# Kernel tuning notes

Measured on AMD Instinct MI355X. Metric: run time of the kernel, lower is better.

## Reference

```python
import jax, jax.numpy as jnp
from jax import lax
import numpy as np

INPUT_SIZE = 128
NUM_FRAMES = 4
NUM_OBJECTS = 32
DN = ('NCHW', 'OIHW', 'NCHW')


def _conv(x, w, b):
    y = lax.conv_general_dilated(x, w, window_strides=(1, 1), padding='SAME',
                                 dimension_numbers=DN)
    return y + b[None, :, None, None]


def setup_inputs() -> dict:
    key = jax.random.key(0)
    k = jax.random.split(key, 6)
    B = 32
    images = jax.random.uniform(k[0], (B, NUM_FRAMES, 3, INPUT_SIZE, INPUT_SIZE), jnp.float32) * 255.0
    rois = jax.random.randint(k[1], (B, INPUT_SIZE, INPUT_SIZE), 0, NUM_OBJECTS, jnp.int32)
    conv1_w = jax.random.normal(k[2], (64, 3 * NUM_FRAMES, 3, 3), jnp.float32) * 0.05
    conv1_b = jnp.zeros((64,), jnp.float32)
    conv2_w = jax.random.normal(k[3], (128, 64, 3, 3), jnp.float32) * 0.05
    conv2_b = jnp.zeros((128,), jnp.float32)
    return {'images': images, 'rois': rois, 'conv1_w': conv1_w, 'conv1_b': conv1_b,
            'conv2_w': conv2_w, 'conv2_b': conv2_b}


def reference(images, rois, conv1_w, conv1_b, conv2_w, conv2_b):
    B = images.shape[0]
    # backbone: conv -> relu -> maxpool2x2 -> conv -> relu
    x = images.reshape(B, 3 * NUM_FRAMES, INPUT_SIZE, INPUT_SIZE) / 255.0
    x = jax.nn.relu(_conv(x, conv1_w, conv1_b))
    x = lax.reduce_window(x, -jnp.inf, lax.max, (1, 1, 2, 2), (1, 1, 2, 2), 'VALID')
    x = jax.nn.relu(_conv(x, conv2_w, conv2_b))  # (B, 128, 64, 64)
    C = x.shape[1]
    # roi_pool: one-hot(rois) nearest-downsampled to 64x64, broadcast-multiply,
    # max over H,W == per-id segment max (x >= 0 post-relu; absent id -> 0)
    ids = rois[:, ::2, ::2].reshape(B, -1)
    feat = x.reshape(B, C, -1).transpose(0, 2, 1)  # (B, HW, C)

    def pool_one(f, i):  # f: (HW, C), i: (HW,)
        return jax.ops.segment_max(f, i, num_segments=NUM_OBJECTS)  # (O, C)

    pooled = jax.vmap(pool_one)(feat, ids)  # (B, O, C)
    return jnp.maximum(pooled, 0.0)
```

## Files before the change

kernel.cpp:

```cpp
#include <hip/hip_runtime.h>

#define IN 128
#define PD 64
#define C1 64
#define C2 128
#define ICC 12
#define NOBJ 32
#define PADW 66

typedef __attribute__((ext_vector_type(8))) short bf16x8;
typedef __attribute__((ext_vector_type(4))) float f32x4;

static __device__ __forceinline__ unsigned short f2bf(float f) {
  unsigned u = __float_as_uint(f);
  return (unsigned short)((u + 0x7FFFu + ((u >> 16) & 1u)) >> 16);
}

__global__ __launch_bounds__(256) void k0_pack_w2(
    const float* __restrict__ w2, unsigned short* __restrict__ wq)
{
  int j = blockIdx.x * 256 + threadIdx.x;
  if (j < 9 * 2 * 8 * 64 * 8) {
    const int e   = j & 7;
    const int l15 = (j >> 3) & 15;
    const int l16 = (j >> 7) & 3;
    const int ocb = (j >> 9) & 7;
    const int k2  = (j >> 12) & 1;
    const int tap = j >> 13;
    const int oc = ocb * 16 + l15;
    const int ic = k2 * 32 + l16 * 8 + e;
    wq[j] = f2bf(w2[((size_t)oc * C1 + ic) * 9 + tap]);
  }
}

__global__ __launch_bounds__(256) void k0_pack_w1(
    const float* __restrict__ w1, unsigned short* __restrict__ wp)
{
  int i = blockIdx.x * 256 + threadIdx.x;
  if (i < 10 * C1 * 16) {
    int tap = i >> 10;
    int rem = i & 1023;
    int oc = rem >> 4, ch = rem & 15;
    float v = (tap < 9 && ch < ICC) ? w1[((size_t)oc * ICC + ch) * 9 + tap] : 0.f;
    wp[i] = f2bf(v);
  }
}

__global__ __launch_bounds__(256) void k_border(unsigned short* __restrict__ xpad)
{
  int i = blockIdx.x * 256 + threadIdx.x;
  if (i >= 32 * 260) return;
  int b = i / 260, p = i - b * 260;
  int y, x;
  if (p < 66)       { y = 0;           x = p; }
  else if (p < 132) { y = 65;          x = p - 66; }
  else if (p < 196) { y = p - 132 + 1; x = 0; }
  else              { y = p - 196 + 1; x = 65; }
  unsigned short* dst = xpad + (((size_t)b * PADW + y) * PADW + x) * C1;
  const uint4 z = make_uint4(0, 0, 0, 0);
#pragma unroll
  for (int k = 0; k < 8; ++k) reinterpret_cast<uint4*>(dst)[k] = z;
}

__global__ __launch_bounds__(512, 6) void k1_mfma(
    const float* __restrict__ img, const unsigned short* __restrict__ wp1,
    const float* __restrict__ b1, unsigned short* __restrict__ xpad)
{
  const int t = threadIdx.x;
  const int l = t & 63, w = t >> 6;
  const int wm = w >> 1, wn = w & 1;
  const int bx = blockIdx.x & 7, by = blockIdx.x >> 3;
  const int b  = blockIdx.y;
  const int l15 = l & 15, l16 = l >> 4;

  __shared__ uint4 xs4[648];

  const float* imgb = img + ((size_t)b * ICC << 14);
  for (int i = t; i < 2592; i += 512) {
    const int cp = i / 324;
    const int pix = i - cp * 324;
    const int y = (pix * 57) >> 10;
    const int x = pix - y * 18;
    const int iy = by * 16 + y - 1, ix = bx * 16 + x - 1;
    unsigned int val = 0;
    if (cp < 6 && iy >= 0 && iy < IN && ix >= 0 && ix < IN) {
      const float* p0 = imgb + ((size_t)(2 * cp) << 14) + iy * IN + ix;
      unsigned short h0 = f2bf(p0[0]     * (1.f / 255.f));
      unsigned short h1 = f2bf(p0[16384] * (1.f / 255.f));
      val = (unsigned int)h0 | ((unsigned int)h1 << 16);
    }
    reinterpret_cast<unsigned int*>(xs4)[pix * 8 + cp] = val;
  }
  __syncthreads();

  f32x4 acc[4][2];
#pragma unroll
  for (int mf = 0; mf < 4; ++mf)
#pragma unroll
    for (int nf = 0; nf < 2; ++nf) acc[mf][nf] = (f32x4){0.f, 0.f, 0.f, 0.f};

  const int ck = l16 & 1;
#pragma unroll
  for (int kp = 0; kp < 5; ++kp) {
    const int ta = 2 * kp, tb = 2 * kp + 1;
    const int tbA = (tb > 8) ? 8 : tb;
    const int dya = ta / 3, dxa = ta % 3;
    const int dyb = tbA / 3, dxb = tbA % 3;
    const int dy = (l16 < 2) ? dya : dyb;
    const int dx = (l16 < 2) ? dxa : dxb;
    const int tw = (l16 < 2) ? ta : tb;

    bf16x8 a[4], bw[2];
#pragma unroll
    for (int mf = 0; mf < 4; ++mf) {
      const int row = wm * 4 + mf;
      a[mf] = *reinterpret_cast<const bf16x8*>(
          &xs4[((row + dy) * 18 + (l15 + dx)) * 2 + ck]);
    }
#pragma unroll
    for (int nf = 0; nf < 2; ++nf) {
      const int oc = wn * 32 + nf * 16 + l15;
      bw[nf] = *reinterpret_cast<const bf16x8*>(wp1 + ((tw * C1 + oc) * 16 + ck * 8));
    }
#pragma unroll
    for (int mf = 0; mf < 4; ++mf)
#pragma unroll
      for (int nf = 0; nf < 2; ++nf)
        acc[mf][nf] = __builtin_amdgcn_mfma_f32_16x16x32_bf16(
            a[mf], bw[nf], acc[mf][nf], 0, 0, 0);
  }

  float bias[2];
#pragma unroll
  for (int nf = 0; nf < 2; ++nf) bias[nf] = b1[wn * 32 + nf * 16 + l15];

#pragma unroll
  for (int q = 0; q < 2; ++q) {
    const int gy = by * 8 + wm * 2 + q;
    unsigned short* orow = xpad + (((size_t)b * PADW + (gy + 1)) * PADW + 1) * C1;
#pragma unroll
    for (int nf = 0; nf < 2; ++nf) {
      const int oc = wn * 32 + nf * 16 + l15;
      const f32x4 A0 = acc[2 * q][nf], A1 = acc[2 * q + 1][nf];
      const float p0 = fmaxf(fmaxf(A0[0], A0[1]), fmaxf(A1[0], A1[1]));
      const float p1 = fmaxf(fmaxf(A0[2], A0[3]), fmaxf(A1[2], A1[3]));
      const float v0 = fmaxf(p0 + bias[nf], 0.f);
      const float v1 = fmaxf(p1 + bias[nf], 0.f);
      const int gx0 = bx * 8 + l16 * 2;
      orow[(size_t)gx0 * C1 + oc]       = f2bf(v0);
      orow[(size_t)(gx0 + 1) * C1 + oc] = f2bf(v1);
    }
  }
}

__global__ __launch_bounds__(256) void k2_mfma(
    const unsigned short* __restrict__ xpad, const unsigned short* __restrict__ wq,
    const float* __restrict__ b2, const int* __restrict__ rois,
    float* __restrict__ part)
{
  const int t  = threadIdx.x;
  const int l  = t & 63, w = t >> 6;
  const int wm = w >> 1, wn = w & 1;
  const int bx = blockIdx.x & 3, by = blockIdx.x >> 2;
  const int b  = blockIdx.y;
  const int l15 = l & 15, l16 = l >> 4;

  __shared__ uint4 xs4[180 * 8];
  __shared__ int   smax[NOBJ * 132];
  __shared__ int   ids_s[128];

  const unsigned short* xb = xpad + (size_t)b * PADW * PADW * C1;
  for (int i = t; i < 1440; i += 256) {
    const int r = i >> 3, ps = i & 7;
    const int y = (r * 57) >> 10;
    const int x = r - y * 18;
    const int cl = ps ^ (r & 7);
    const int gy = by * 8 + y, gx = bx * 16 + x;
    xs4[i] = *(reinterpret_cast<const uint4*>(xb + ((size_t)gy * PADW + gx) * C1) + cl);
  }
  if (t < 128) {
    const int py = t >> 4, pxx = t & 15;
    ids_s[t] = rois[((size_t)b * IN + 2 * (by * 8 + py)) * IN + 2 * (bx * 16 + pxx)];
  }
  {
    uint4* sm4 = reinterpret_cast<uint4*>(smax);
    const uint4 z = make_uint4(0, 0, 0, 0);
#pragma unroll
    for (int i = 0; i < 5; ++i) {
      const int j = t + i * 256;
      if (j < 1056) sm4[j] = z;
    }
  }
  __syncthreads();

  f32x4 acc[4][4];
#pragma unroll
  for (int mf = 0; mf < 4; ++mf)
#pragma unroll
    for (int nf = 0; nf < 4; ++nf) acc[mf][nf] = (f32x4){0.f, 0.f, 0.f, 0.f};

  const char* xs_raw = reinterpret_cast<const char*>(xs4);

  bf16x8 aR[2][4], bR[2][4];
#pragma unroll
  for (int mf = 0; mf < 4; ++mf) {
    const int m_loc = wm * 64 + mf * 16 + l15;
    const int s = (m_loc >> 4) * 18 + (m_loc & 15);
    const int c = l16 ^ (s & 7);
    aR[0][mf] = *reinterpret_cast<const bf16x8*>(xs_raw + s * 128 + c * 16);
  }
#pragma unroll
  for (int nf = 0; nf < 4; ++nf)
    bR[0][nf] = *reinterpret_cast<const bf16x8*>(
        wq + ((size_t)(wn * 4 + nf)) * 512 + l * 8);

#pragma unroll
  for (int st = 0; st < 18; ++st) {
    const int cur = st & 1, nxt = cur ^ 1;
    if (st < 17) {
      const int s1 = st + 1;
      const int tap1 = s1 >> 1, k21 = s1 & 1;
      const int kr1 = tap1 / 3, kc1 = tap1 % 3;
#pragma unroll
      for (int mf = 0; mf < 4; ++mf) {
        const int m_loc = wm * 64 + mf * 16 + l15;
        const int s = ((m_loc >> 4) + kr1) * 18 + ((m_loc & 15) + kc1);
        const int c = (k21 * 4 + l16) ^ (s & 7);
        aR[nxt][mf] = *reinterpret_cast<const bf16x8*>(xs_raw + s * 128 + c * 16);
      }
#pragma unroll
      for (int nf = 0; nf < 4; ++nf)
        bR[nxt][nf] = *reinterpret_cast<const bf16x8*>(
            wq + ((size_t)((tap1 * 2 + k21) * 8 + wn * 4 + nf)) * 512 + l * 8);
    }
#pragma unroll
    for (int mf = 0; mf < 4; ++mf)
#pragma unroll
      for (int nf = 0; nf < 4; ++nf)
        acc[mf][nf] = __builtin_amdgcn_mfma_f32_16x16x32_bf16(
            aR[cur][mf], bR[cur][nf], acc[mf][nf], 0, 0, 0);
  }

  float bias[4];
#pragma unroll
  for (int nf = 0; nf < 4; ++nf) bias[nf] = b2[wn * 64 + nf * 16 + l15];

#pragma unroll
  for (int mf = 0; mf < 4; ++mf) {
#pragma unroll
    for (int reg = 0; reg < 4; ++reg) {
      const int m_loc = wm * 64 + mf * 16 + l16 * 4 + reg;
      const int id = ids_s[m_loc];
#pragma unroll
      for (int nf = 0; nf < 4; ++nf) {
        const int oc = wn * 64 + nf * 16 + l15;
        const float val = fmaxf(acc[mf][nf][reg] + bias[nf], 0.f);
        atomicMax(&smax[id * 132 + oc], __float_as_int(val));
      }
    }
  }
  __syncthreads();

  uint4* pb4 = reinterpret_cast<uint4*>(part + ((size_t)b * 32 + blockIdx.x) * (NOBJ * C2));
  const uint4* sm4 = reinterpret_cast<const uint4*>(smax);
#pragma unroll
  for (int i = 0; i < 4; ++i) {
    const int j = t + i * 256;
    const int row = j >> 5, c4 = j & 31;
    pb4[j] = sm4[row * 33 + c4];
  }
}

__global__ __launch_bounds__(256) void k3_reduce(
    const float* __restrict__ part, float* __restrict__ out)
{
  const int idx = blockIdx.x * 256 + threadIdx.x;
  const int b = idx >> 12, slot = idx & 4095;
  const float* p = part + (size_t)b * 32 * 4096 + slot;
  float m = 0.f;
#pragma unroll
  for (int tl = 0; tl < 32; ++tl) m = fmaxf(m, p[tl * 4096]);
  out[idx] = m;
}

extern "C" void kernel_launch(void* const* d_in, const int* in_sizes, int n_in,
                              void* d_out, int out_size, void* d_ws, size_t ws_size,
                              hipStream_t stream)
{
  (void)in_sizes; (void)n_in; (void)ws_size; (void)out_size;
  const float* images = (const float*)d_in[0];
  const int*   rois   = (const int*)d_in[1];
  const float* w1     = (const float*)d_in[2];
  const float* b1     = (const float*)d_in[3];
  const float* w2     = (const float*)d_in[4];
  const float* b2     = (const float*)d_in[5];

  const size_t xpad_bytes = (size_t)32 * PADW * PADW * C1 * 2;
  const size_t wq_bytes   = (size_t)9 * 2 * 8 * 64 * 8 * 2;
  const size_t wp1_bytes  = (size_t)10 * C1 * 16 * 2;

  unsigned short* xpad = (unsigned short*)d_ws;
  unsigned short* wq   = (unsigned short*)((char*)d_ws + xpad_bytes);
  unsigned short* wp1  = (unsigned short*)((char*)d_ws + xpad_bytes + wq_bytes);
  float* part = (float*)((char*)d_ws + xpad_bytes + wq_bytes + wp1_bytes);

  hipLaunchKernelGGL(k_border, dim3(33), dim3(256), 0, stream, xpad);
  hipLaunchKernelGGL(k0_pack_w2, dim3(288), dim3(256), 0, stream, w2, wq);
  hipLaunchKernelGGL(k0_pack_w1, dim3(40),  dim3(256), 0, stream, w1, wp1);

  hipLaunchKernelGGL(k1_mfma, dim3(64, 32), dim3(512), 0, stream,
                     images, wp1, b1, xpad);

  hipLaunchKernelGGL(k2_mfma, dim3(32, 32), dim3(256), 0, stream,
                     xpad, wq, b2, rois, part);

  hipLaunchKernelGGL(k3_reduce, dim3(512), dim3(256), 0, stream,
                     part, (float*)d_out);
}
```

Baseline: 63.97 us.

## Fuse weight packing and border zeroing into conv kernels, drop prep launches

Removes the three small prep kernels (border zeroing, conv1 weight pack, conv2 weight pack). Conv1 weights are now converted to bf16 inside each conv1 block and staged in LDS. Conv2 packing runs in an extra row of conv1 blocks, and conv2 masks out-of-range padded pixels to zero instead of relying on a pre-zeroed border. This saves launch overhead at the cost of redundant per-block weight conversion, more LDS per block, and lower occupancy in conv1 (launch bound 6 to 4).

```diff
diff --git a/kernel.cpp b/kernel.cpp
--- a/kernel.cpp
+++ b/kernel.cpp
@@ -16,57 +16,24 @@
   return (unsigned short)((u + 0x7FFFu + ((u >> 16) & 1u)) >> 16);
 }
 
-__global__ __launch_bounds__(256) void k0_pack_w2(
-    const float* __restrict__ w2, unsigned short* __restrict__ wq)
-{
-  int j = blockIdx.x * 256 + threadIdx.x;
-  if (j < 9 * 2 * 8 * 64 * 8) {
-    const int e   = j & 7;
-    const int l15 = (j >> 3) & 15;
-    const int l16 = (j >> 7) & 3;
-    const int ocb = (j >> 9) & 7;
-    const int k2  = (j >> 12) & 1;
-    const int tap = j >> 13;
-    const int oc = ocb * 16 + l15;
-    const int ic = k2 * 32 + l16 * 8 + e;
-    wq[j] = f2bf(w2[((size_t)oc * C1 + ic) * 9 + tap]);
-  }
-}
-
-__global__ __launch_bounds__(256) void k0_pack_w1(
-    const float* __restrict__ w1, unsigned short* __restrict__ wp)
-{
-  int i = blockIdx.x * 256 + threadIdx.x;
-  if (i < 10 * C1 * 16) {
-    int tap = i >> 10;
-    int rem = i & 1023;
-    int oc = rem >> 4, ch = rem & 15;
-    float v = (tap < 9 && ch < ICC) ? w1[((size_t)oc * ICC + ch) * 9 + tap] : 0.f;
-    wp[i] = f2bf(v);
-  }
-}
-
-__global__ __launch_bounds__(256) void k_border(unsigned short* __restrict__ xpad)
-{
-  int i = blockIdx.x * 256 + threadIdx.x;
-  if (i >= 32 * 260) return;
-  int b = i / 260, p = i - b * 260;
-  int y, x;
-  if (p < 66)       { y = 0;           x = p; }
-  else if (p < 132) { y = 65;          x = p - 66; }
-  else if (p < 196) { y = p - 132 + 1; x = 0; }
-  else              { y = p - 196 + 1; x = 65; }
-  unsigned short* dst = xpad + (((size_t)b * PADW + y) * PADW + x) * C1;
-  const uint4 z = make_uint4(0, 0, 0, 0);
-#pragma unroll
-  for (int k = 0; k < 8; ++k) reinterpret_cast<uint4*>(dst)[k] = z;
-}
-
-__global__ __launch_bounds__(512, 6) void k1_mfma(
-    const float* __restrict__ img, const unsigned short* __restrict__ wp1,
-    const float* __restrict__ b1, unsigned short* __restrict__ xpad)
+__global__ __launch_bounds__(512, 4) void k1_mfma(
+    const float* __restrict__ img, const float* __restrict__ w1,
+    const float* __restrict__ b1, const float* __restrict__ w2,
+    unsigned short* __restrict__ wq, unsigned short* __restrict__ xpad)
 {
   const int t = threadIdx.x;
+
+  if (blockIdx.y == 32) {
+    for (int j = blockIdx.x * 512 + t; j < 9 * C2 * C1; j += 64 * 512) {
+      const int tmp = j / 9, tap = j - tmp * 9;
+      const int ic = tmp & 63, oc = tmp >> 6;
+      const int k2 = ic >> 5, l16 = (ic >> 3) & 3, e = ic & 7;
+      const int ocb = oc >> 4, l15 = oc & 15;
+      wq[((tap * 2 + k2) * 8 + ocb) * 512 + l16 * 128 + l15 * 8 + e] = f2bf(w2[j]);
+    }
+    return;
+  }
+
   const int l = t & 63, w = t >> 6;
   const int wm = w >> 1, wn = w & 1;
   const int bx = blockIdx.x & 7, by = blockIdx.x >> 3;
@@ -74,6 +41,24 @@
   const int l15 = l & 15, l16 = l >> 4;
 
   __shared__ uint4 xs4[648];
+  __shared__ uint4 lds_w4[1920];
+  unsigned short* lds_w = reinterpret_cast<unsigned short*>(lds_w4);
+
+  {
+    const uint4 z = make_uint4(0, 0, 0, 0);
+#pragma unroll
+    for (int i = 0; i < 4; ++i) {
+      const int j = t + i * 512;
+      if (j < 1920) lds_w4[j] = z;
+    }
+  }
+  __syncthreads();
+
+  for (int j = t; j < C1 * ICC * 9; j += 512) {
+    const int tmp = j / 9, tap = j - tmp * 9;
+    const int ch = tmp % ICC, oc = tmp / ICC;
+    lds_w[(tap * C1 + oc) * 24 + ch] = f2bf(w1[j]);
+  }
 
   const float* imgb = img + ((size_t)b * ICC << 14);
   for (int i = t; i < 2592; i += 512) {
@@ -120,7 +105,7 @@
 #pragma unroll
     for (int nf = 0; nf < 2; ++nf) {
       const int oc = wn * 32 + nf * 16 + l15;
-      bw[nf] = *reinterpret_cast<const bf16x8*>(wp1 + ((tw * C1 + oc) * 16 + ck * 8));
+      bw[nf] = *reinterpret_cast<const bf16x8*>(&lds_w[(tw * C1 + oc) * 24 + ck * 8]);
     }
 #pragma unroll
     for (int mf = 0; mf < 4; ++mf)
@@ -176,7 +161,10 @@
     const int x = r - y * 18;
     const int cl = ps ^ (r & 7);
     const int gy = by * 8 + y, gx = bx * 16 + x;
-    xs4[i] = *(reinterpret_cast<const uint4*>(xb + ((size_t)gy * PADW + gx) * C1) + cl);
+    uint4 v = make_uint4(0, 0, 0, 0);
+    if (gy >= 1 && gy <= PD && gx >= 1 && gx <= PD)
+      v = *(reinterpret_cast<const uint4*>(xb + ((size_t)gy * PADW + gx) * C1) + cl);
+    xs4[i] = v;
   }
   if (t < 128) {
     const int py = t >> 4, pxx = t & 15;
@@ -222,16 +210,16 @@
       const int tap1 = s1 >> 1, k21 = s1 & 1;
       const int kr1 = tap1 / 3, kc1 = tap1 % 3;
 #pragma unroll
+      for (int nf = 0; nf < 4; ++nf)
+        bR[nxt][nf] = *reinterpret_cast<const bf16x8*>(
+            wq + ((size_t)((tap1 * 2 + k21) * 8 + wn * 4 + nf)) * 512 + l * 8);
+#pragma unroll
       for (int mf = 0; mf < 4; ++mf) {
         const int m_loc = wm * 64 + mf * 16 + l15;
         const int s = ((m_loc >> 4) + kr1) * 18 + ((m_loc & 15) + kc1);
         const int c = (k21 * 4 + l16) ^ (s & 7);
         aR[nxt][mf] = *reinterpret_cast<const bf16x8*>(xs_raw + s * 128 + c * 16);
       }
-#pragma unroll
-      for (int nf = 0; nf < 4; ++nf)
-        bR[nxt][nf] = *reinterpret_cast<const bf16x8*>(
-            wq + ((size_t)((tap1 * 2 + k21) * 8 + wn * 4 + nf)) * 512 + l * 8);
     }
 #pragma unroll
     for (int mf = 0; mf < 4; ++mf)
@@ -296,20 +284,14 @@
   const float* b2     = (const float*)d_in[5];
 
   const size_t xpad_bytes = (size_t)32 * PADW * PADW * C1 * 2;
-  const size_t wq_bytes   = (size_t)9 * 2 * 8 * 64 * 8 * 2;
-  const size_t wp1_bytes  = (size_t)10 * C1 * 16 * 2;
+  const size_t wq_bytes   = (size_t)9 * C2 * C1 * 2;
 
   unsigned short* xpad = (unsigned short*)d_ws;
   unsigned short* wq   = (unsigned short*)((char*)d_ws + xpad_bytes);
-  unsigned short* wp1  = (unsigned short*)((char*)d_ws + xpad_bytes + wq_bytes);
-  float* part = (float*)((char*)d_ws + xpad_bytes + wq_bytes + wp1_bytes);
-
-  hipLaunchKernelGGL(k_border, dim3(33), dim3(256), 0, stream, xpad);
-  hipLaunchKernelGGL(k0_pack_w2, dim3(288), dim3(256), 0, stream, w2, wq);
-  hipLaunchKernelGGL(k0_pack_w1, dim3(40),  dim3(256), 0, stream, w1, wp1);
-
-  hipLaunchKernelGGL(k1_mfma, dim3(64, 32), dim3(512), 0, stream,
-                     images, wp1, b1, xpad);
+  float* part = (float*)((char*)d_ws + xpad_bytes + wq_bytes);
+
+  hipLaunchKernelGGL(k1_mfma, dim3(64, 33), dim3(512), 0, stream,
+                     images, w1, b1, w2, wq, xpad);
 
   hipLaunchKernelGGL(k2_mfma, dim3(32, 32), dim3(256), 0, stream,
                      xpad, wq, b2, rois, part);
```

Result: no change. 63.41 us (-0.9%).
